# Kernel optimization log

Hardware: AMD Instinct MI355X
Metric: run time of the kernel (lower is better)

The kernel has to match this reference:

```python
import jax, jax.numpy as jnp
import numpy as np

H = W = 128
R = 2
H2, W2 = H // R, W // R
TOPK = 3
NSEG = H * W + 1  # segment 0 = background


def _ccl(binary):
    """8-connected component labeling via iterative max-label propagation.
    binary: [H,W] bool. Returns int32 labels, 0 = background; each component
    gets a unique (arbitrary) positive id = max pixel index in the component."""
    idx = jnp.arange(1, H * W + 1, dtype=jnp.int32).reshape(H, W)
    lab0 = jnp.where(binary, idx, 0)

    def cond(c):
        return c[1]

    def body(c):
        lab, _ = c
        nb = jax.lax.reduce_window(lab, jnp.int32(0), jax.lax.max,
                                   (3, 3), (1, 1), 'SAME')  # 3x3 incl. self
        new = jnp.where(binary, nb, 0)
        return new, jnp.any(new != lab)

    lab, _ = jax.lax.while_loop(cond, body, (lab0, jnp.bool_(True)))
    return lab


def _process_one(prob_i, feat_i):
    """prob_i: [1,H,W], feat_i: [Cf,H,W] -> [3*Cf, H2, W2]."""
    p = prob_i[0]
    binary = p > 0.5
    lab = _ccl(binary).reshape(-1)  # [H*W] segment ids

    ones = jnp.ones((H * W,), jnp.float32)
    count = jax.ops.segment_sum(ones, lab, num_segments=NSEG)
    conf_sum = jax.ops.segment_sum(p.reshape(-1), lab, num_segments=NSEG)
    mean_conf = conf_sum / jnp.maximum(count, 1.0)

    rows = jnp.repeat(jnp.arange(H, dtype=jnp.int32), W)
    cols = jnp.tile(jnp.arange(W, dtype=jnp.int32), H)
    min_r = jax.ops.segment_min(rows, lab, num_segments=NSEG)
    max_r = jax.ops.segment_max(rows, lab, num_segments=NSEG)
    min_c = jax.ops.segment_min(cols, lab, num_segments=NSEG)
    max_c = jax.ops.segment_max(cols, lab, num_segments=NSEG)

    valid = (count > 0) & (jnp.arange(NSEG) > 0)
    score = jnp.where(valid, mean_conf, -jnp.inf)
    _, top_idx = jax.lax.top_k(score, TOPK)  # regions sorted by mean confidence
    K = jnp.sum(valid.astype(jnp.int32))     # number of connected regions

    # duplication rules: K==0 -> full image x3; K==1 -> [f0,f0,f0];
    # K==2 -> [f0,f0,f1]; K>=3 -> [f0,f1,f2]
    i0, i1 = top_idx[0], top_idx[1]
    slots = jnp.where(K >= 3, top_idx,
            jnp.where(K == 2, jnp.stack([i0, i0, i1]),
                      jnp.stack([i0, i0, i0])))

    mr = jnp.where(K > 0, min_r[slots], 0)
    Mr = jnp.where(K > 0, max_r[slots] + 1, H)  # bbox half-open, regionprops style
    mc = jnp.where(K > 0, min_c[slots], 0)
    Mc = jnp.where(K > 0, max_c[slots] + 1, W)

    def crop(a, b, c, d):
        # PyTorch nearest interpolate: src = floor(dst * in/out)
        r = a + (jnp.arange(H2) * (b - a)) // H2
        cc = c + (jnp.arange(W2) * (d - c)) // W2
        return feat_i[:, r][:, :, cc]  # [Cf, H2, W2]

    out = jax.vmap(crop)(mr, Mr, mc, Mc)  # [3, Cf, H2, W2]
    return out.reshape(-1, H2, W2)         # [3*Cf, H2, W2]


def setup_inputs() -> dict:
    key = jax.random.key(0)
    k1, k2 = jax.random.split(key)
    prob = jax.random.uniform(k1, (16, 1, H, W), dtype=jnp.float32)
    feat = jax.random.normal(k2, (16, 192, H, W), dtype=jnp.float32)
    return {"prob": prob, "feat": feat}


def reference(prob, feat):
    return jax.vmap(_process_one)(prob, feat)  # [B, 3*Cf, H2, W2]
```

## Files before the change

### kernel.cpp

```cpp
#include <hip/hip_runtime.h>
#include <limits.h>

#define HH 128
#define WW_ 128
#define HW 16384
#define NB 16
#define CF 192
#define H2 64
#define W2 64

#define SH 16
#define NSPI 8
#define NST 128
#define SC 512
#define NCI 4096
#define NLRUN 1024

typedef float vf4 __attribute__((ext_vector_type(4)));
typedef unsigned long long ull;


__device__ inline int uf_find(int* par, int x) {
    volatile int* vp = (volatile int*)par;
    int p = vp[x];
    while (p != x) {
        int g = vp[p];
        vp[x] = g;
        x = g;
        p = vp[x];
    }
    return x;
}

__device__ inline void uf_union(int* par, int a, int b) {
    int ra = uf_find(par, a);
    int rb = uf_find(par, b);
    while (ra != rb) {
        if (ra < rb) { int t = ra; ra = rb; rb = t; }
        int old = atomicCAS(&par[ra], ra, rb);
        if (old == ra) return;
        ra = uf_find(par, old);
        rb = uf_find(par, rb);
    }
}


__device__ inline int getbit2(ull lo, ull hi, int c) {
    return (int)(((c < 64) ? (lo >> c) : (hi >> (c - 64))) & 1ULL);
}

__device__ inline int leading_ones(ull v) {
    ull nv = ~v;
    return (nv == 0ULL) ? 64 : __clzll(nv);
}

__device__ inline int trailing_ones(ull v) {
    ull nv = ~v;
    return (nv == 0ULL) ? 64 : (__ffsll(nv) - 1);
}

__device__ inline int run_start_col(ull lo, ull hi, int c) {
    if (c < 64) {
        int ones = leading_ones(lo << (63 - c));
        return c - ones + 1;
    }
    int ones = leading_ones(hi << (127 - c));
    int rs = c - ones + 1;
    if (rs == 64) rs -= leading_ones(lo);
    return rs;
}

__device__ inline int run_index(ull rs_lo, ull rs_hi, int cs) {
    if (cs < 64)  return __popcll(rs_lo & ((1ULL << cs) - 1ULL));
    if (cs == 64) return __popcll(rs_lo);
    return __popcll(rs_lo) + __popcll(rs_hi & ((1ULL << (cs - 64)) - 1ULL));
}

__device__ inline void top3_ins(float s, int id, int x,
    float& s0, float& s1, float& s2,
    int& i0, int& i1, int& i2,
    int& x0, int& x1, int& x2)
{
    if (x < 0) return;
    if (s > s0 || (s == s0 && id < i0)) {
        s2 = s1; i2 = i1; x2 = x1;
        s1 = s0; i1 = i0; x1 = x0;
        s0 = s;  i0 = id; x0 = x;
    } else if (s > s1 || (s == s1 && id < i1)) {
        s2 = s1; i2 = i1; x2 = x1;
        s1 = s;  i1 = id; x1 = x;
    } else if (s > s2 || (s == s2 && id < i2)) {
        s2 = s;  i2 = id; x2 = x;
    }
}


__global__ __launch_bounds__(256) void stripe_ccl(
    const float* __restrict__ prob,
    int* __restrict__ nlocg, int* __restrict__ gcnt, float* __restrict__ gconf,
    int* __restrict__ gminr, int* __restrict__ gmaxr,
    int* __restrict__ gminc, int* __restrict__ gmaxc,
    int* __restrict__ gmaxid, int* __restrict__ brun, ull* __restrict__ bmask)
{
    __shared__ ull rowm[SH][2];
    __shared__ unsigned char m8[256];
    __shared__ int parent[NLRUN];
    __shared__ int   lcnt[SC];
    __shared__ float lconf[SC];
    __shared__ int lminr[SC], lmaxr[SC], lminc[SC], lmaxc[SC], lmaxid[SC];
    __shared__ int snloc;

    const int g = blockIdx.x;
    const int b = g >> 3, s = g & 7;
    const int row0 = s * SH;
    const int tid = threadIdx.x;
    const int row = tid >> 4;
    const int w0 = (tid & 15) * 8;

    if (tid == 0) snloc = 0;

    const float* p = prob + (size_t)b * HW + (size_t)((row0 + row) << 7) + w0;
    vf4 va = *(const vf4*)p;
    vf4 vb = *(const vf4*)(p + 4);
    int mask8 = 0;
    mask8 |= (va.x > 0.5f) << 0; mask8 |= (va.y > 0.5f) << 1;
    mask8 |= (va.z > 0.5f) << 2; mask8 |= (va.w > 0.5f) << 3;
    mask8 |= (vb.x > 0.5f) << 4; mask8 |= (vb.y > 0.5f) << 5;
    mask8 |= (vb.z > 0.5f) << 6; mask8 |= (vb.w > 0.5f) << 7;
    m8[tid] = (unsigned char)mask8;
    for (int j = tid; j < SC; j += 256) {
        lcnt[j] = 0; lconf[j] = 0.f;
        lminr[j] = INT_MAX; lmaxr[j] = -1;
        lminc[j] = INT_MAX; lmaxc[j] = -1;
        lmaxid[j] = 0;
    }
    __syncthreads();
    if (tid < 32) {
        int r = tid >> 1, half = tid & 1;
        ull v = 0;
        #pragma unroll
        for (int k2 = 0; k2 < 8; ++k2)
            v |= (ull)m8[(r << 4) + (half << 3) + k2] << (k2 * 8);
        rowm[r][half] = v;
    }
    __syncthreads();

    for (int rid = tid; rid < NLRUN; rid += 256) {
        int r = rid >> 6;
        ull lo = rowm[r][0], hi = rowm[r][1];
        ull rs_lo = lo & ~(lo << 1);
        ull rs_hi = hi & ~((hi << 1) | (lo >> 63));
        int nruns = __popcll(rs_lo) + __popcll(rs_hi);
        if ((rid & 63) < nruns) parent[rid] = rid;
    }
    __syncthreads();

    for (int i = tid; i < (SH - 1) * 128; i += 256) {
        int r = 1 + (i >> 7), c = i & 127;
        ull lo = rowm[r][0], hi = rowm[r][1];
        if (!getbit2(lo, hi, c)) continue;
        ull ulo = rowm[r - 1][0], uhi = rowm[r - 1][1];
        int l  = (c > 0)   ? getbit2(lo, hi, c - 1) : 0;
        int rt = (c < 127) ? getbit2(lo, hi, c + 1) : 0;
        int up = getbit2(ulo, uhi, c);
        int ul = (c > 0)   ? getbit2(ulo, uhi, c - 1) : 0;
        int ur = (c < 127) ? getbit2(ulo, uhi, c + 1) : 0;
        bool u1 = up && !(l && ul);
        bool u2 = !up && ul && !l;
        bool u3 = !up && ur && !rt;
        if (!(u1 | u2 | u3)) continue;
        ull rs_lo = lo & ~(lo << 1),   rs_hi = hi & ~((hi << 1) | (lo >> 63));
        ull urs_lo = ulo & ~(ulo << 1), urs_hi = uhi & ~((uhi << 1) | (ulo >> 63));
        int cs = run_start_col(lo, hi, c);
        int rid = (r << 6) + run_index(rs_lo, rs_hi, cs);
        int ub = (r - 1) << 6;
        if (u1) uf_union(parent, rid, ub + run_index(urs_lo, urs_hi, run_start_col(ulo, uhi, c)));
        if (u2) uf_union(parent, rid, ub + run_index(urs_lo, urs_hi, run_start_col(ulo, uhi, c - 1)));
        if (u3) uf_union(parent, rid, ub + run_index(urs_lo, urs_hi, run_start_col(ulo, uhi, c + 1)));
    }
    __syncthreads();

    for (int rid = tid; rid < NLRUN; rid += 256) {
        int r = rid >> 6;
        ull lo = rowm[r][0], hi = rowm[r][1];
        ull rs_lo = lo & ~(lo << 1);
        ull rs_hi = hi & ~((hi << 1) | (lo >> 63));
        int nruns = __popcll(rs_lo) + __popcll(rs_hi);
        if ((rid & 63) < nruns) parent[rid] = uf_find(parent, rid);
    }
    __syncthreads();
    for (int rid = tid; rid < NLRUN; rid += 256) {
        int r = rid >> 6;
        ull lo = rowm[r][0], hi = rowm[r][1];
        ull rs_lo = lo & ~(lo << 1);
        ull rs_hi = hi & ~((hi << 1) | (lo >> 63));
        int nruns = __popcll(rs_lo) + __popcll(rs_hi);
        if ((rid & 63) < nruns && parent[rid] == rid) {
            int idx = atomicAdd(&snloc, 1);
            parent[rid] = NLRUN + idx;
        }
    }
    __syncthreads();

    {
        ull lo = rowm[row][0], hi = rowm[row][1];
        ull rs_lo = lo & ~(lo << 1);
        ull rs_hi = hi & ~((hi << 1) | (lo >> 63));
        const float vv[8] = {va.x, va.y, va.z, va.w, vb.x, vb.y, vb.z, vb.w};
        const int imr = row0 + row;
        int curIdx = -1, aCnt = 0, aMinc = 0, aMaxc = 0, aMaxid = 0;
        float aConf = 0.f;
        bool prevfg = false;
        #pragma unroll
        for (int j = 0; j < 8; ++j) {
            bool fg = (mask8 >> j) & 1;
            if (fg) {
                int c = w0 + j;
                if (!prevfg) {
                    int cs = run_start_col(lo, hi, c);
                    int rid = (row << 6) + run_index(rs_lo, rs_hi, cs);
                    int v = parent[rid];
                    int idx = (v >= NLRUN) ? v - NLRUN : parent[v] - NLRUN;
                    if (idx != curIdx) {
                        if (curIdx >= 0) {
                            atomicAdd(&lcnt[curIdx], aCnt);
                            atomicAdd(&lconf[curIdx], aConf);
                            atomicMin(&lminr[curIdx], imr);
                            atomicMax(&lmaxr[curIdx], imr);
                            atomicMin(&lminc[curIdx], aMinc);
                            atomicMax(&lmaxc[curIdx], aMaxc);
                            atomicMax(&lmaxid[curIdx], aMaxid);
                        }
                        curIdx = idx; aCnt = 0; aConf = 0.f;
                        aMinc = c; aMaxc = c; aMaxid = 0;
                    }
                }
                aCnt++; aConf += vv[j]; aMaxc = c;
                aMaxid = (imr << 7) + c + 1;
            }
            prevfg = fg;
        }
        if (curIdx >= 0) {
            atomicAdd(&lcnt[curIdx], aCnt);
            atomicAdd(&lconf[curIdx], aConf);
            atomicMin(&lminr[curIdx], imr);
            atomicMax(&lmaxr[curIdx], imr);
            atomicMin(&lminc[curIdx], aMinc);
            atomicMax(&lmaxc[curIdx], aMaxc);
            atomicMax(&lmaxid[curIdx], aMaxid);
        }
    }
    __syncthreads();

    const int nl = snloc;
    for (int j = tid; j < nl; j += 256) {
        int d = (g << 9) + j;
        gcnt[d] = lcnt[j];  gconf[d] = lconf[j];
        gminr[d] = lminr[j]; gmaxr[d] = lmaxr[j];
        gminc[d] = lminc[j]; gmaxc[d] = lmaxc[j];
        gmaxid[d] = lmaxid[j];
    }
    if (tid == 0) nlocg[g] = nl;
    if (tid < 128) {
        int br = tid >> 6;
        int j = tid & 63;
        int r = br ? (SH - 1) : 0;
        ull lo = rowm[r][0], hi = rowm[r][1];
        ull rs_lo = lo & ~(lo << 1);
        ull rs_hi = hi & ~((hi << 1) | (lo >> 63));
        int nruns = __popcll(rs_lo) + __popcll(rs_hi);
        if (j < nruns) {
            int rid = (r << 6) + j;
            int v = parent[rid];
            brun[(g << 7) + (br << 6) + j] = (v >= NLRUN) ? v - NLRUN : parent[v] - NLRUN;
        }
        if (j == 0) {
            bmask[(g << 2) + (br << 1) + 0] = lo;
            bmask[(g << 2) + (br << 1) + 1] = hi;
        }
    }
}


__global__ __launch_bounds__(1024) void merge_kernel(
    const int* __restrict__ nlocg, const int* __restrict__ gcnt,
    const float* __restrict__ gconf,
    const int* __restrict__ gminr, const int* __restrict__ gmaxr,
    const int* __restrict__ gminc, const int* __restrict__ gmaxc,
    const int* __restrict__ gmaxid, const int* __restrict__ brun,
    const ull* __restrict__ bmask, int* __restrict__ bbox)
{
    __shared__ int parent2[NCI];
    __shared__ int   cnt2[NCI];
    __shared__ float conf2[NCI];
    __shared__ int minr2[NCI], maxr2[NCI], minc2[NCI], maxc2[NCI], maxid2[NCI];
    __shared__ int sK;
    __shared__ float wss[48];
    __shared__ int wid_[48], wrx[48];

    const int b = blockIdx.x;
    const int tid = threadIdx.x;
    if (tid == 0) sK = 0;
    for (int i = tid; i < NCI; i += 1024) { parent2[i] = i; cnt2[i] = 0; }
    __syncthreads();

    for (int s = 0; s < NSPI; ++s) {
        int g = (b << 3) + s;
        int n = nlocg[g];
        for (int j = tid; j < n; j += 1024) {
            int d = (s << 9) + j, e = (g << 9) + j;
            cnt2[d] = gcnt[e];  conf2[d] = gconf[e];
            minr2[d] = gminr[e]; maxr2[d] = gmaxr[e];
            minc2[d] = gminc[e]; maxc2[d] = gmaxc[e];
            maxid2[d] = gmaxid[e];
        }
    }
    __syncthreads();

    for (int i = tid; i < 7 * 128; i += 1024) {
        int k = 1 + (i >> 7), c = i & 127;
        int gLo = (b << 3) + k, gUp = gLo - 1;
        ull lo = bmask[(gLo << 2) + 0], hi = bmask[(gLo << 2) + 1];
        if (!getbit2(lo, hi, c)) continue;
        ull ulo = bmask[(gUp << 2) + 2], uhi = bmask[(gUp << 2) + 3];
        int l  = (c > 0)   ? getbit2(lo, hi, c - 1) : 0;
        int rt = (c < 127) ? getbit2(lo, hi, c + 1) : 0;
        int up = getbit2(ulo, uhi, c);
        int ul = (c > 0)   ? getbit2(ulo, uhi, c - 1) : 0;
        int ur = (c < 127) ? getbit2(ulo, uhi, c + 1) : 0;
        bool u1 = up && !(l && ul);
        bool u2 = !up && ul && !l;
        bool u3 = !up && ur && !rt;
        if (!(u1 | u2 | u3)) continue;
        ull rs_lo = lo & ~(lo << 1),   rs_hi = hi & ~((hi << 1) | (lo >> 63));
        ull urs_lo = ulo & ~(ulo << 1), urs_hi = uhi & ~((uhi << 1) | (ulo >> 63));
        int cs = run_start_col(lo, hi, c);
        int myid = (k << 9) + brun[(gLo << 7) + run_index(rs_lo, rs_hi, cs)];
        int ubase = (k - 1) << 9;
        if (u1) uf_union(parent2, myid, ubase + brun[(gUp << 7) + 64 + run_index(urs_lo, urs_hi, run_start_col(ulo, uhi, c))]);
        if (u2) uf_union(parent2, myid, ubase + brun[(gUp << 7) + 64 + run_index(urs_lo, urs_hi, run_start_col(ulo, uhi, c - 1))]);
        if (u3) uf_union(parent2, myid, ubase + brun[(gUp << 7) + 64 + run_index(urs_lo, urs_hi, run_start_col(ulo, uhi, c + 1))]);
    }
    __syncthreads();

    for (int i = tid; i < NCI; i += 1024) {
        if (cnt2[i] > 0) {
            int r = uf_find(parent2, i);
            if (r != i) {
                atomicAdd(&cnt2[r], cnt2[i]);   atomicAdd(&conf2[r], conf2[i]);
                atomicMin(&minr2[r], minr2[i]); atomicMax(&maxr2[r], maxr2[i]);
                atomicMin(&minc2[r], minc2[i]); atomicMax(&maxc2[r], maxc2[i]);
                atomicMax(&maxid2[r], maxid2[i]);
            }
        }
    }
    __syncthreads();

    float s0 = -INFINITY, s1 = -INFINITY, s2 = -INFINITY;
    int i0 = INT_MAX, i1 = INT_MAX, i2 = INT_MAX;
    int x0 = -1, x1 = -1, x2 = -1;
    int kc = 0;
    for (int i = tid; i < NCI; i += 1024) {
        if (parent2[i] == i && cnt2[i] > 0) {
            ++kc;
            float sc = conf2[i] / (float)cnt2[i];
            top3_ins(sc, maxid2[i], i, s0, s1, s2, i0, i1, i2, x0, x1, x2);
        }
    }
    for (int off = 32; off; off >>= 1) kc += __shfl_xor(kc, off);
    if ((tid & 63) == 0) atomicAdd(&sK, kc);
    for (int off = 32; off; off >>= 1) {
        float bs0 = __shfl_xor(s0, off), bs1 = __shfl_xor(s1, off), bs2 = __shfl_xor(s2, off);
        int bi0 = __shfl_xor(i0, off), bi1 = __shfl_xor(i1, off), bi2 = __shfl_xor(i2, off);
        int bx0 = __shfl_xor(x0, off), bx1 = __shfl_xor(x1, off), bx2 = __shfl_xor(x2, off);
        top3_ins(bs0, bi0, bx0, s0, s1, s2, i0, i1, i2, x0, x1, x2);
        top3_ins(bs1, bi1, bx1, s0, s1, s2, i0, i1, i2, x0, x1, x2);
        top3_ins(bs2, bi2, bx2, s0, s1, s2, i0, i1, i2, x0, x1, x2);
    }
    if ((tid & 63) == 0) {
        int w = tid >> 6;
        wss[w * 3 + 0] = s0; wid_[w * 3 + 0] = i0; wrx[w * 3 + 0] = x0;
        wss[w * 3 + 1] = s1; wid_[w * 3 + 1] = i1; wrx[w * 3 + 1] = x1;
        wss[w * 3 + 2] = s2; wid_[w * 3 + 2] = i2; wrx[w * 3 + 2] = x2;
    }
    __syncthreads();

    if (tid == 0) {
        float t0 = -INFINITY, t1 = -INFINITY, t2 = -INFINITY;
        int ti0 = INT_MAX, ti1 = INT_MAX, ti2 = INT_MAX;
        int tx0 = -1, tx1 = -1, tx2 = -1;
        for (int t = 0; t < 48; ++t)
            top3_ins(wss[t], wid_[t], wrx[t], t0, t1, t2, ti0, ti1, ti2, tx0, tx1, tx2);
        int K = sK;
        int roots[3];
        if (K >= 3)      { roots[0] = tx0; roots[1] = tx1; roots[2] = tx2; }
        else if (K == 2) { roots[0] = tx0; roots[1] = tx0; roots[2] = tx1; }
        else             { roots[0] = tx0; roots[1] = tx0; roots[2] = tx0; }
        for (int slot = 0; slot < 3; ++slot) {
            int mr, h, mc, w;
            if (K == 0) { mr = 0; h = HH; mc = 0; w = WW_; }
            else {
                int rt = roots[slot];
                mr = minr2[rt]; h = maxr2[rt] + 1 - mr;
                mc = minc2[rt]; w = maxc2[rt] + 1 - mc;
            }
            int* o = bbox + (b * 3 + slot) * 4;
            o[0] = mr; o[1] = h; o[2] = mc; o[3] = w;
        }
    }
}


__global__ __launch_bounds__(256) void crop_kernel(
    const float* __restrict__ feat, const int* __restrict__ bbox,
    float* __restrict__ out)
{
    const int gid = blockIdx.x * 256 + threadIdx.x;
    const int x4 = gid & 15;
    const int y  = (gid >> 4) & 63;
    const int t  = gid >> 10;
    const int c  = t % CF;
    const int bs = t / CF;
    const int* bb = bbox + bs * 4;
    const int mr = bb[0], h = bb[1], mc = bb[2], w = bb[3];
    const int r = mr + ((y * h) >> 6);
    const int bimg = bs / 3;
    const float* row = feat + (((size_t)bimg * CF + c) * HH + r) * WW_;
    const int x = x4 * 4;
    vf4 v;
    v.x = row[mc + (((x + 0) * w) >> 6)];
    v.y = row[mc + (((x + 1) * w) >> 6)];
    v.z = row[mc + (((x + 2) * w) >> 6)];
    v.w = row[mc + (((x + 3) * w) >> 6)];
    __builtin_nontemporal_store(v, (vf4*)out + gid);
}


extern "C" void kernel_launch(void* const* d_in, const int* in_sizes, int n_in,
                              void* d_out, int out_size, void* d_ws, size_t ws_size,
                              hipStream_t stream) {
    const float* prob = (const float*)d_in[0];
    const float* feat = (const float*)d_in[1];
    float* out = (float*)d_out;

    int* ws = (int*)d_ws;
    int* bbox   = ws;
    int* nlocg  = ws + 192;
    int* gcnt   = ws + 320;
    float* gconf = (float*)(ws + 320 + 1 * 65536);
    int* gminr  = ws + 320 + 2 * 65536;
    int* gmaxr  = ws + 320 + 3 * 65536;
    int* gminc  = ws + 320 + 4 * 65536;
    int* gmaxc  = ws + 320 + 5 * 65536;
    int* gmaxid = ws + 320 + 6 * 65536;
    int* brun   = ws + 320 + 7 * 65536;
    ull* bmask  = (ull*)(ws + 320 + 7 * 65536 + 16384);

    hipLaunchKernelGGL(stripe_ccl, dim3(NST), dim3(256), 0, stream,
                       prob, nlocg, gcnt, gconf, gminr, gmaxr, gminc, gmaxc,
                       gmaxid, brun, bmask);
    hipLaunchKernelGGL(merge_kernel, dim3(NB), dim3(1024), 0, stream,
                       nlocg, gcnt, gconf, gminr, gmaxr, gminc, gmaxc,
                       gmaxid, brun, bmask, bbox);
    const int total4 = NB * 3 * CF * H2 * (W2 / 4);
    hipLaunchKernelGGL(crop_kernel, dim3(total4 / 256), dim3(256), 0, stream,
                       feat, bbox, out);
}
```

Baseline: 351.7 us.

## Fuse per-image merge into stripe CCL via last-block atomic counter; coarsen crop kernel

The separate merge kernel is removed. The last stripe block to finish each image, found through an atomic counter with release/acquire ordering, merges the stripe boundaries and does top-3 selection. The per-region statistics are reduced with global atomics in place rather than being copied into shared memory. The crop kernel now uses 1024-thread blocks that each process four output vectors. This saves a kernel launch and the shared-memory staging, but adds a memset and puts the merge on a single 256-thread block per image.

```diff
diff --git a/kernel.cpp b/kernel.cpp
--- a/kernel.cpp
+++ b/kernel.cpp
@@ -15,6 +15,8 @@
 #define SC 512
 #define NCI 4096
 #define NLRUN 1024
+
+#define CROP_BLKS 2304
 
 typedef float vf4 __attribute__((ext_vector_type(4)));
 typedef unsigned long long ull;
@@ -52,11 +54,6 @@
 __device__ inline int leading_ones(ull v) {
     ull nv = ~v;
     return (nv == 0ULL) ? 64 : __clzll(nv);
-}
-
-__device__ inline int trailing_ones(ull v) {
-    ull nv = ~v;
-    return (nv == 0ULL) ? 64 : (__ffsll(nv) - 1);
 }
 
 __device__ inline int run_start_col(ull lo, ull hi, int c) {
@@ -94,13 +91,21 @@
     }
 }
 
-
-__global__ __launch_bounds__(256) void stripe_ccl(
+__device__ inline int aload(const int* p) {
+    return __hip_atomic_load(p, __ATOMIC_RELAXED, __HIP_MEMORY_SCOPE_AGENT);
+}
+__device__ inline float aloadf(const float* p) {
+    return __hip_atomic_load(p, __ATOMIC_RELAXED, __HIP_MEMORY_SCOPE_AGENT);
+}
+
+
+__global__ __launch_bounds__(256) void stripe_ccl_merge(
     const float* __restrict__ prob,
     int* __restrict__ nlocg, int* __restrict__ gcnt, float* __restrict__ gconf,
     int* __restrict__ gminr, int* __restrict__ gmaxr,
     int* __restrict__ gminc, int* __restrict__ gmaxc,
-    int* __restrict__ gmaxid, int* __restrict__ brun, ull* __restrict__ bmask)
+    int* __restrict__ gmaxid, int* __restrict__ brun, ull* __restrict__ bmask,
+    int* __restrict__ imgcnt, int* __restrict__ bbox)
 {
     __shared__ ull rowm[SH][2];
     __shared__ unsigned char m8[256];
@@ -109,6 +114,11 @@
     __shared__ float lconf[SC];
     __shared__ int lminr[SC], lmaxr[SC], lminc[SC], lmaxc[SC], lmaxid[SC];
     __shared__ int snloc;
+    __shared__ int parent2[NCI];
+    __shared__ int nl8[NSPI];
+    __shared__ int sLast, sK;
+    __shared__ float wss[12];
+    __shared__ int wid_[12], wrx[12];
 
     const int g = blockIdx.x;
     const int b = g >> 3, s = g & 7;
@@ -279,45 +289,25 @@
             bmask[(g << 2) + (br << 1) + 1] = hi;
         }
     }
-}
-
-
-__global__ __launch_bounds__(1024) void merge_kernel(
-    const int* __restrict__ nlocg, const int* __restrict__ gcnt,
-    const float* __restrict__ gconf,
-    const int* __restrict__ gminr, const int* __restrict__ gmaxr,
-    const int* __restrict__ gminc, const int* __restrict__ gmaxc,
-    const int* __restrict__ gmaxid, const int* __restrict__ brun,
-    const ull* __restrict__ bmask, int* __restrict__ bbox)
-{
-    __shared__ int parent2[NCI];
-    __shared__ int   cnt2[NCI];
-    __shared__ float conf2[NCI];
-    __shared__ int minr2[NCI], maxr2[NCI], minc2[NCI], maxc2[NCI], maxid2[NCI];
-    __shared__ int sK;
-    __shared__ float wss[48];
-    __shared__ int wid_[48], wrx[48];
-
-    const int b = blockIdx.x;
-    const int tid = threadIdx.x;
-    if (tid == 0) sK = 0;
-    for (int i = tid; i < NCI; i += 1024) { parent2[i] = i; cnt2[i] = 0; }
-    __syncthreads();
-
-    for (int s = 0; s < NSPI; ++s) {
-        int g = (b << 3) + s;
-        int n = nlocg[g];
-        for (int j = tid; j < n; j += 1024) {
-            int d = (s << 9) + j, e = (g << 9) + j;
-            cnt2[d] = gcnt[e];  conf2[d] = gconf[e];
-            minr2[d] = gminr[e]; maxr2[d] = gmaxr[e];
-            minc2[d] = gminc[e]; maxc2[d] = gmaxc[e];
-            maxid2[d] = gmaxid[e];
-        }
-    }
-    __syncthreads();
-
-    for (int i = tid; i < 7 * 128; i += 1024) {
+    __syncthreads();
+
+    if (tid == 0) {
+        int old = __hip_atomic_fetch_add(&imgcnt[b], 1,
+                      __ATOMIC_RELEASE, __HIP_MEMORY_SCOPE_AGENT);
+        int last = (old == NSPI - 1);
+        if (last)
+            (void)__hip_atomic_load(&imgcnt[b],
+                      __ATOMIC_ACQUIRE, __HIP_MEMORY_SCOPE_AGENT);
+        sLast = last; sK = 0;
+    }
+    __syncthreads();
+    if (!sLast) return;
+
+    for (int i = tid; i < NCI; i += 256) parent2[i] = i;
+    if (tid < NSPI) nl8[tid] = nlocg[(b << 3) + tid];
+    __syncthreads();
+
+    for (int i = tid; i < 7 * 128; i += 256) {
         int k = 1 + (i >> 7), c = i & 127;
         int gLo = (b << 3) + k, gUp = gLo - 1;
         ull lo = bmask[(gLo << 2) + 0], hi = bmask[(gLo << 2) + 1];
@@ -343,45 +333,54 @@
     }
     __syncthreads();
 
-    for (int i = tid; i < NCI; i += 1024) {
-        if (cnt2[i] > 0) {
+    const int hb = b << 12;
+    for (int s2 = 0; s2 < NSPI; ++s2) {
+        for (int j = tid; j < nl8[s2]; j += 256) {
+            int i = (s2 << 9) + j;
             int r = uf_find(parent2, i);
             if (r != i) {
-                atomicAdd(&cnt2[r], cnt2[i]);   atomicAdd(&conf2[r], conf2[i]);
-                atomicMin(&minr2[r], minr2[i]); atomicMax(&maxr2[r], maxr2[i]);
-                atomicMin(&minc2[r], minc2[i]); atomicMax(&maxc2[r], maxc2[i]);
-                atomicMax(&maxid2[r], maxid2[i]);
+                atomicAdd(&gcnt[hb + r], gcnt[hb + i]);
+                atomicAdd(&gconf[hb + r], gconf[hb + i]);
+                atomicMin(&gminr[hb + r], gminr[hb + i]);
+                atomicMax(&gmaxr[hb + r], gmaxr[hb + i]);
+                atomicMin(&gminc[hb + r], gminc[hb + i]);
+                atomicMax(&gmaxc[hb + r], gmaxc[hb + i]);
+                atomicMax(&gmaxid[hb + r], gmaxid[hb + i]);
             }
         }
     }
     __syncthreads();
 
-    float s0 = -INFINITY, s1 = -INFINITY, s2 = -INFINITY;
+    float s0 = -INFINITY, s1 = -INFINITY, s2v = -INFINITY;
     int i0 = INT_MAX, i1 = INT_MAX, i2 = INT_MAX;
     int x0 = -1, x1 = -1, x2 = -1;
     int kc = 0;
-    for (int i = tid; i < NCI; i += 1024) {
-        if (parent2[i] == i && cnt2[i] > 0) {
-            ++kc;
-            float sc = conf2[i] / (float)cnt2[i];
-            top3_ins(sc, maxid2[i], i, s0, s1, s2, i0, i1, i2, x0, x1, x2);
+    for (int s2 = 0; s2 < NSPI; ++s2) {
+        for (int j = tid; j < nl8[s2]; j += 256) {
+            int i = (s2 << 9) + j;
+            if (parent2[i] == i) {
+                ++kc;
+                float sc = aloadf(&gconf[hb + i]) / (float)aload(&gcnt[hb + i]);
+                top3_ins(sc, aload(&gmaxid[hb + i]), i,
+                         s0, s1, s2v, i0, i1, i2, x0, x1, x2);
+            }
         }
     }
     for (int off = 32; off; off >>= 1) kc += __shfl_xor(kc, off);
     if ((tid & 63) == 0) atomicAdd(&sK, kc);
     for (int off = 32; off; off >>= 1) {
-        float bs0 = __shfl_xor(s0, off), bs1 = __shfl_xor(s1, off), bs2 = __shfl_xor(s2, off);
+        float bs0 = __shfl_xor(s0, off), bs1 = __shfl_xor(s1, off), bs2 = __shfl_xor(s2v, off);
         int bi0 = __shfl_xor(i0, off), bi1 = __shfl_xor(i1, off), bi2 = __shfl_xor(i2, off);
         int bx0 = __shfl_xor(x0, off), bx1 = __shfl_xor(x1, off), bx2 = __shfl_xor(x2, off);
-        top3_ins(bs0, bi0, bx0, s0, s1, s2, i0, i1, i2, x0, x1, x2);
-        top3_ins(bs1, bi1, bx1, s0, s1, s2, i0, i1, i2, x0, x1, x2);
-        top3_ins(bs2, bi2, bx2, s0, s1, s2, i0, i1, i2, x0, x1, x2);
+        top3_ins(bs0, bi0, bx0, s0, s1, s2v, i0, i1, i2, x0, x1, x2);
+        top3_ins(bs1, bi1, bx1, s0, s1, s2v, i0, i1, i2, x0, x1, x2);
+        top3_ins(bs2, bi2, bx2, s0, s1, s2v, i0, i1, i2, x0, x1, x2);
     }
     if ((tid & 63) == 0) {
         int w = tid >> 6;
         wss[w * 3 + 0] = s0; wid_[w * 3 + 0] = i0; wrx[w * 3 + 0] = x0;
         wss[w * 3 + 1] = s1; wid_[w * 3 + 1] = i1; wrx[w * 3 + 1] = x1;
-        wss[w * 3 + 2] = s2; wid_[w * 3 + 2] = i2; wrx[w * 3 + 2] = x2;
+        wss[w * 3 + 2] = s2v; wid_[w * 3 + 2] = i2; wrx[w * 3 + 2] = x2;
     }
     __syncthreads();
 
@@ -389,7 +388,7 @@
         float t0 = -INFINITY, t1 = -INFINITY, t2 = -INFINITY;
         int ti0 = INT_MAX, ti1 = INT_MAX, ti2 = INT_MAX;
         int tx0 = -1, tx1 = -1, tx2 = -1;
-        for (int t = 0; t < 48; ++t)
+        for (int t = 0; t < 12; ++t)
             top3_ins(wss[t], wid_[t], wrx[t], t0, t1, t2, ti0, ti1, ti2, tx0, tx1, tx2);
         int K = sK;
         int roots[3];
@@ -401,8 +400,8 @@
             if (K == 0) { mr = 0; h = HH; mc = 0; w = WW_; }
             else {
                 int rt = roots[slot];
-                mr = minr2[rt]; h = maxr2[rt] + 1 - mr;
-                mc = minc2[rt]; w = maxc2[rt] + 1 - mc;
+                mr = aload(&gminr[hb + rt]); h = aload(&gmaxr[hb + rt]) + 1 - mr;
+                mc = aload(&gminc[hb + rt]); w = aload(&gmaxc[hb + rt]) + 1 - mc;
             }
             int* o = bbox + (b * 3 + slot) * 4;
             o[0] = mr; o[1] = h; o[2] = mc; o[3] = w;
@@ -411,28 +410,32 @@
 }
 
 
-__global__ __launch_bounds__(256) void crop_kernel(
+__global__ __launch_bounds__(1024) void crop_kernel(
     const float* __restrict__ feat, const int* __restrict__ bbox,
     float* __restrict__ out)
 {
-    const int gid = blockIdx.x * 256 + threadIdx.x;
-    const int x4 = gid & 15;
-    const int y  = (gid >> 4) & 63;
-    const int t  = gid >> 10;
-    const int c  = t % CF;
-    const int bs = t / CF;
-    const int* bb = bbox + bs * 4;
-    const int mr = bb[0], h = bb[1], mc = bb[2], w = bb[3];
-    const int r = mr + ((y * h) >> 6);
-    const int bimg = bs / 3;
-    const float* row = feat + (((size_t)bimg * CF + c) * HH + r) * WW_;
-    const int x = x4 * 4;
-    vf4 v;
-    v.x = row[mc + (((x + 0) * w) >> 6)];
-    v.y = row[mc + (((x + 1) * w) >> 6)];
-    v.z = row[mc + (((x + 2) * w) >> 6)];
-    v.w = row[mc + (((x + 3) * w) >> 6)];
-    __builtin_nontemporal_store(v, (vf4*)out + gid);
+    const int base = blockIdx.x * 1024 + threadIdx.x;
+    #pragma unroll
+    for (int k = 0; k < 4; ++k) {
+        const int gid = base + k * (CROP_BLKS * 1024);
+        const int x4 = gid & 15;
+        const int y  = (gid >> 4) & 63;
+        const int t  = gid >> 10;
+        const int c  = t % CF;
+        const int bs = t / CF;
+        const int* bb = bbox + bs * 4;
+        const int mr = bb[0], h = bb[1], mc = bb[2], w = bb[3];
+        const int r = mr + ((y * h) >> 6);
+        const int bimg = bs / 3;
+        const float* row = feat + (((size_t)bimg * CF + c) * HH + r) * WW_;
+        const int x = x4 * 4;
+        vf4 v;
+        v.x = row[mc + (((x + 0) * w) >> 6)];
+        v.y = row[mc + (((x + 1) * w) >> 6)];
+        v.z = row[mc + (((x + 2) * w) >> 6)];
+        v.w = row[mc + (((x + 3) * w) >> 6)];
+        __builtin_nontemporal_store(v, (vf4*)out + gid);
+    }
 }
 
 
@@ -455,14 +458,13 @@
     int* gmaxid = ws + 320 + 6 * 65536;
     int* brun   = ws + 320 + 7 * 65536;
     ull* bmask  = (ull*)(ws + 320 + 7 * 65536 + 16384);
-
-    hipLaunchKernelGGL(stripe_ccl, dim3(NST), dim3(256), 0, stream,
+    int* imgcnt = ws + 320 + 7 * 65536 + 16384 + 1024;
+
+    hipMemsetAsync(imgcnt, 0, NB * sizeof(int), stream);
+
+    hipLaunchKernelGGL(stripe_ccl_merge, dim3(NST), dim3(256), 0, stream,
                        prob, nlocg, gcnt, gconf, gminr, gmaxr, gminc, gmaxc,
-                       gmaxid, brun, bmask);
-    hipLaunchKernelGGL(merge_kernel, dim3(NB), dim3(1024), 0, stream,
-                       nlocg, gcnt, gconf, gminr, gmaxr, gminc, gmaxc,
-                       gmaxid, brun, bmask, bbox);
-    const int total4 = NB * 3 * CF * H2 * (W2 / 4);
-    hipLaunchKernelGGL(crop_kernel, dim3(total4 / 256), dim3(256), 0, stream,
+                       gmaxid, brun, bmask, imgcnt, bbox);
+    hipLaunchKernelGGL(crop_kernel, dim3(CROP_BLKS), dim3(1024), 0, stream,
                        feat, bbox, out);
 }
```

After: 371.5 us. 1.06x slower.
